# Kernel optimization log

Hardware: AMD Instinct MI355X
Metric: run time of the kernel (lower is better)

Reference implementation:

```python
import jax, jax.numpy as jnp
import numpy as np

M, NM, EM = 7, 1024, 32768        # modules, nodes/module, edges/module
N, E = M * NM, M * EM
F, D, H = 128, 64, 4              # node feats, hidden_channels, heads
HC = H * D


def setup_inputs() -> dict:
    key = jax.random.key(0)
    ks = jax.random.split(key, 20)
    x = jax.random.normal(ks[0], (N, F), jnp.float32)
    # intra-module edges; nodes of module m occupy [m*NM, (m+1)*NM)
    base = jnp.repeat(jnp.arange(M, dtype=jnp.int32) * NM, EM)
    src = base + jax.random.randint(ks[1], (E,), 0, NM, dtype=jnp.int32)
    dst = base + jax.random.randint(ks[2], (E,), 0, NM, dtype=jnp.int32)
    edge_index = jnp.stack([src, dst])
    module_assignments = jnp.repeat(jnp.arange(M, dtype=jnp.int32), NM)
    rn = lambda k, sh: jax.random.normal(k, sh, jnp.float32) * 0.05
    return dict(
        x=x, edge_index=edge_index, module_assignments=module_assignments,
        g1_w=rn(ks[3], (M, F, H, D)), g1_as=rn(ks[4], (M, H, D)), g1_ad=rn(ks[5], (M, H, D)),
        g1_b=jnp.zeros((M, HC), jnp.float32),
        g2_w=rn(ks[6], (M, HC, 1, D)), g2_as=rn(ks[7], (M, 1, D)), g2_ad=rn(ks[8], (M, 1, D)),
        g2_b=jnp.zeros((M, D), jnp.float32),
        sa_in_w=rn(ks[9], (M, 3 * D, D)), sa_in_b=jnp.zeros((M, 3 * D), jnp.float32),
        sa_out_w=rn(ks[10], (M, D, D)), sa_out_b=jnp.zeros((M, D), jnp.float32),
        ca_in_w=rn(ks[11], (3 * D, D)), ca_in_b=jnp.zeros((3 * D,), jnp.float32),
        ca_out_w=rn(ks[12], (D, D)), ca_out_b=jnp.zeros((D,), jnp.float32),
        fusion_w=jnp.ones((M,), jnp.float32) / M,
        fc_w=rn(ks[13], (M * D, D)), fc_b=jnp.zeros((D,), jnp.float32),
        c1_w=rn(ks[14], (D, D // 2)), c1_b=jnp.zeros((D // 2,), jnp.float32),
        c2_w=rn(ks[15], (D // 2, 2)), c2_b=jnp.zeros((2,), jnp.float32))


def _gat(x, src, dst, W, a_s, a_d, b, concat):
    # PyG-style GATConv (eval mode, add_self_loops=True). x:[NM,Fin], W:[Fin,h,c]
    h = jnp.einsum('nf,fhc->nhc', x, W)          # [NM,h,c]
    es = (h * a_s).sum(-1)                        # [NM,h]
    ed = (h * a_d).sum(-1)
    sl = jnp.arange(NM, dtype=src.dtype)
    s = jnp.concatenate([src, sl])                # add self-loops
    d = jnp.concatenate([dst, sl])
    e = jax.nn.leaky_relu(es[s] + ed[d], 0.2)     # [E+NM,h]
    mx = jax.ops.segment_max(e, d, num_segments=NM)
    ex = jnp.exp(e - mx[d])
    den = jax.ops.segment_sum(ex, d, num_segments=NM)
    alpha = ex / (den[d] + 1e-16)
    out = jax.ops.segment_sum(alpha[:, :, None] * h[s], d, num_segments=NM)  # [NM,h,c]
    out = out.reshape(NM, -1) if concat else out.mean(axis=1)
    return out + b


def _mha(x, in_w, in_b, out_w, out_b, nh):
    # torch nn.MultiheadAttention, batch_first, batch=1, eval mode
    L, d = x.shape
    dh = d // nh
    q, k, v = jnp.split(x @ in_w.T + in_b, 3, axis=-1)
    q = q.reshape(L, nh, dh); k = k.reshape(L, nh, dh); v = v.reshape(L, nh, dh)
    att = jax.nn.softmax(jnp.einsum('qhd,khd->hqk', q, k) * (1.0 / np.sqrt(dh)), axis=-1)
    o = jnp.einsum('hqk,khd->qhd', att, v).reshape(L, d)
    return o @ out_w.T + out_b


def _forward(x, edge_index, g1_w, g1_as, g1_ad, g1_b, g2_w, g2_as, g2_ad, g2_b,
             sa_in_w, sa_in_b, sa_out_w, sa_out_b, ca_in_w, ca_in_b, ca_out_w, ca_out_b,
             fusion_w, fc_w, fc_b, c1_w, c1_b, c2_w, c2_b):
    # per-module subgraph extraction + reindex: modules are contiguous node
    # blocks and edges are grouped per module, so mask/relabel is a reshape.
    ei = edge_index.reshape(2, M, EM)
    offs = (jnp.arange(M, dtype=ei.dtype) * NM)[:, None]
    src = ei[0] - offs                 # [M,EM] local indices
    dst = ei[1] - offs
    xm = x.reshape(M, NM, F)

    def per_module(xm_, s_, d_, g1w, g1a, g1d, g1b_, g2w_, g2a, g2d, g2b_, siw, sib, sow, sob):
        h = jax.nn.relu(_gat(xm_, s_, d_, g1w, g1a, g1d, g1b_, True))   # [NM,HC]
        h = jax.nn.relu(_gat(h, s_, d_, g2w_, g2a, g2d, g2b_, False))   # [NM,D]
        h = _mha(h, siw, sib, sow, sob, H)                              # module self-attention
        return h.mean(axis=0)                                            # [D]

    reps = jax.vmap(per_module)(xm, src, dst, g1_w, g1_as, g1_ad, g1_b,
                                g2_w, g2_as, g2_ad, g2_b,
                                sa_in_w, sa_in_b, sa_out_w, sa_out_b)    # [M,D]
    cross = _mha(reps, ca_in_w, ca_in_b, ca_out_w, ca_out_b, H)          # [M,D]
    w = jax.nn.softmax(fusion_w)
    fused = (cross * w[:, None]).reshape(1, M * D) @ fc_w + fc_b         # [1,D]
    out = jax.nn.relu(fused @ c1_w + c1_b) @ c2_w + c2_b                 # [1,2]
    return out, reps


def reference(x, edge_index, module_assignments, g1_w, g1_as, g1_ad, g1_b,
              g2_w, g2_as, g2_ad, g2_b, sa_in_w, sa_in_b, sa_out_w, sa_out_b,
              ca_in_w, ca_in_b, ca_out_w, ca_out_b, fusion_w, fc_w, fc_b,
              c1_w, c1_b, c2_w, c2_b):
    del module_assignments  # encoded as contiguous blocks of NM nodes per module
    return _forward(x, edge_index, g1_w, g1_as, g1_ad, g1_b, g2_w, g2_as, g2_ad, g2_b,
                    sa_in_w, sa_in_b, sa_out_w, sa_out_b, ca_in_w, ca_in_b, ca_out_w,
                    ca_out_b, fusion_w, fc_w, fc_b, c1_w, c1_b, c2_w, c2_b)
```

## Files before the change

### kernel.cpp

```cpp
#include <hip/hip_runtime.h>
#include <hip/hip_bf16.h>
#include <stdint.h>

#define MODS 7
#define NMOD 1024
#define EMOD 32768
#define NN (MODS*NMOD)
#define EE (MODS*EMOD)
#define KC2 4
#define G1B (MODS*16*4)
#define NCHUNK 32

typedef __hip_bfloat16 bf16;

static __device__ __forceinline__ float lrelu(float x){ return x > 0.f ? x : 0.2f*x; }
static __device__ __forceinline__ float bfu(unsigned short u){ return __uint_as_float(((unsigned)u) << 16); }
static __device__ __forceinline__ float2 f2fma(float2 a, float2 b, float2 c){
  return make_float2(fmaf(a.x,b.x,c.x), fmaf(a.y,b.y,c.y));
}

template<int K, int JT, bool TB, int RT, bool OBF, int SC, bool TRQ>
__device__ __forceinline__ void gemm_body(int b, const float* __restrict__ A,
    const float* __restrict__ B, const float* __restrict__ bias, void* __restrict__ Cv,
    const float* __restrict__ a_s, const float* __restrict__ a_d,
    float* __restrict__ es, float* __restrict__ ed) {
  constexpr int jt = JT/64;
  constexpr int rtiles = NMOD/RT;
  constexpr int RPT = RT/16;
  int ct = b % jt; b /= jt;
  int rt = b % rtiles; b /= rtiles;
  int m = b;
  int row0 = m*NMOD + rt*RT;
  int col0 = ct*64;
  __shared__ float Ast[32][RT+4];
  __shared__ float Bs[32][68];
  float acc[RPT][4] = {};
  int tid = threadIdx.x;
  int tr = (tid >> 4) * RPT;
  int tc = (tid & 15) * 4;
  const float* Bm = B + (size_t)m*K*JT;
  for (int k0 = 0; k0 < K; k0 += 32) {
    if constexpr (RT >= 32) {
      constexpr int ANUM = RT*32/1024;
      #pragma unroll
      for (int i = 0; i < ANUM; ++i) {
        int it = tid + i*256;
        int rr = it >> 3, kk0 = (it & 7)*4;
        float4 t = *(const float4*)&A[(size_t)(row0+rr)*K + k0 + kk0];
        Ast[kk0+0][rr] = t.x; Ast[kk0+1][rr] = t.y; Ast[kk0+2][rr] = t.z; Ast[kk0+3][rr] = t.w;
      }
    } else {
      if (tid < 128) {
        int rr = tid >> 3, kk0 = (tid & 7)*4;
        float4 t = *(const float4*)&A[(size_t)(row0+rr)*K + k0 + kk0];
        Ast[kk0+0][rr] = t.x; Ast[kk0+1][rr] = t.y; Ast[kk0+2][rr] = t.z; Ast[kk0+3][rr] = t.w;
      }
    }
    #pragma unroll
    for (int i = 0; i < 2; ++i) {
      int it = tid + i*256;
      if (!TB) {
        int kk = it >> 4, jj0 = (it & 15)*4;
        float4 t = *(const float4*)&Bm[(size_t)(k0+kk)*JT + col0 + jj0];
        Bs[kk][jj0] = t.x; Bs[kk][jj0+1] = t.y; Bs[kk][jj0+2] = t.z; Bs[kk][jj0+3] = t.w;
      } else {
        int jj = it >> 3, kk0 = (it & 7)*4;
        float4 t = *(const float4*)&Bm[(size_t)(col0+jj)*K + k0 + kk0];
        Bs[kk0+0][jj] = t.x; Bs[kk0+1][jj] = t.y; Bs[kk0+2][jj] = t.z; Bs[kk0+3][jj] = t.w;
      }
    }
    __syncthreads();
    #pragma unroll
    for (int kk = 0; kk < 32; ++kk) {
      float4 bv = *(const float4*)&Bs[kk][tc];
      float av[RPT];
      if constexpr (RPT == 4) {
        float4 t = *(const float4*)&Ast[kk][tr];
        av[0] = t.x; av[1] = t.y; av[2] = t.z; av[3] = t.w;
      } else if constexpr (RPT == 2) {
        av[0] = Ast[kk][tr]; av[1] = Ast[kk][tr+1];
      } else {
        av[0] = Ast[kk][tr];
      }
      #pragma unroll
      for (int i = 0; i < RPT; ++i) {
        acc[i][0] += av[i]*bv.x; acc[i][1] += av[i]*bv.y;
        acc[i][2] += av[i]*bv.z; acc[i][3] += av[i]*bv.w;
      }
    }
    __syncthreads();
  }
  float4 bb = {0,0,0,0};
  if (bias) bb = *(const float4*)&bias[m*JT + col0 + tc];
  #pragma unroll
  for (int i = 0; i < RPT; ++i) {
    float4 o = { acc[i][0]+bb.x, acc[i][1]+bb.y, acc[i][2]+bb.z, acc[i][3]+bb.w };
    if constexpr (TRQ) {
      float* Cp = (float*)Cv;
      size_t idx = ((size_t)(m*3 + ct)*NMOD + (rt*RT + tr + i))*64 + tc;
      *(float4*)&Cp[idx] = o;
    } else {
      size_t idx = (size_t)(row0+tr+i)*JT + col0 + tc;
      if constexpr (OBF) {
        bf16* Cp = (bf16*)Cv;
        bf16 tmp[4] = { __float2bfloat16(o.x), __float2bfloat16(o.y),
                        __float2bfloat16(o.z), __float2bfloat16(o.w) };
        *(uint2*)&Cp[idx] = *(const uint2*)tmp;
      } else {
        float* Cp = (float*)Cv;
        *(float4*)&Cp[idx] = o;
      }
    }
  }
  if constexpr (SC == 4) {
    int hh = ct;
    float4 as4 = *(const float4*)&a_s[(m*4 + hh)*64 + tc];
    float4 ad4 = *(const float4*)&a_d[(m*4 + hh)*64 + tc];
    #pragma unroll
    for (int i = 0; i < RPT; ++i) {
      float s = acc[i][0]*as4.x + acc[i][1]*as4.y + acc[i][2]*as4.z + acc[i][3]*as4.w;
      float d = acc[i][0]*ad4.x + acc[i][1]*ad4.y + acc[i][2]*ad4.z + acc[i][3]*ad4.w;
      #pragma unroll
      for (int off = 1; off < 16; off <<= 1) { s += __shfl_xor(s, off); d += __shfl_xor(d, off); }
      if ((tid & 15) == 0) {
        es[(row0+tr+i)*4 + hh] = s;
        ed[(row0+tr+i)*4 + hh] = d;
      }
    }
  }
  if constexpr (SC == 1) {
    float4 as4 = *(const float4*)&a_s[m*64 + tc];
    float4 ad4 = *(const float4*)&a_d[m*64 + tc];
    float s = acc[0][0]*as4.x + acc[0][1]*as4.y + acc[0][2]*as4.z + acc[0][3]*as4.w;
    float d = acc[0][0]*ad4.x + acc[0][1]*ad4.y + acc[0][2]*ad4.z + acc[0][3]*ad4.w;
    #pragma unroll
    for (int off = 1; off < 16; off <<= 1) { s += __shfl_xor(s, off); d += __shfl_xor(d, off); }
    if ((tid & 15) == 0) { es[row0+tr] = s; ed[row0+tr] = d; }
  }
}

__device__ __forceinline__ void hist_body(int mm, const int* __restrict__ dst,
                                          int* __restrict__ rs, int* __restrict__ rs2) {
  __shared__ int hc[NMOD];
  __shared__ int hws[4];
  int tid = threadIdx.x;
  hc[tid] = 0; hc[tid+256] = 0; hc[tid+512] = 0; hc[tid+768] = 0;
  __syncthreads();
  const int4* d4 = (const int4*)(dst + mm*EMOD);
  int base = mm*NMOD;
  for (int it = tid; it < EMOD/4; it += 256) {
    int4 d = d4[it];
    atomicAdd(&hc[d.x - base], 1); atomicAdd(&hc[d.y - base], 1);
    atomicAdd(&hc[d.z - base], 1); atomicAdd(&hc[d.w - base], 1);
  }
  __syncthreads();
  int lane = tid & 63, wid = tid >> 6;
  int i0 = tid*4;
  int v0 = hc[i0], v1 = hc[i0+1], v2 = hc[i0+2], v3 = hc[i0+3];
  int T = v0+v1+v2+v3;
  int X = T;
  #pragma unroll
  for (int off = 1; off < 64; off <<= 1) { int t = __shfl_up(X, off); if (lane >= off) X += t; }
  if (lane == 63) hws[wid] = X;
  __syncthreads();
  int woff = 0;
  #pragma unroll
  for (int w = 0; w < 4; ++w) if (w < wid) woff += hws[w];
  int ex = mm*EMOD + woff + X - T;
  int4 o = make_int4(ex, ex+v0, ex+v0+v1, ex+v0+v1+v2);
  *(int4*)&rs[base + i0]  = o;
  *(int4*)&rs2[base + i0] = o;
  if (mm == MODS-1 && tid == 255) rs[NN] = EE;
}

__global__ __launch_bounds__(256) void k_g1h(const float* __restrict__ x,
    const float* __restrict__ g1w, bf16* __restrict__ h1,
    const float* __restrict__ a_s, const float* __restrict__ a_d,
    float* __restrict__ es, float* __restrict__ ed,
    const int* __restrict__ dst, int* __restrict__ rs, int* __restrict__ rs2) {
  if (blockIdx.x < G1B)
    gemm_body<128,256,false,64,true,4,false>(blockIdx.x, x, g1w, nullptr, h1, a_s, a_d, es, ed);
  else
    hist_body(blockIdx.x - G1B, dst, rs, rs2);
}

__global__ __launch_bounds__(256) void k_g2s(const float* __restrict__ A,
    const float* __restrict__ B, bf16* __restrict__ h2,
    const float* __restrict__ a_s, const float* __restrict__ a_d,
    float* __restrict__ es, float* __restrict__ ed) {
  gemm_body<256,64,false,16,true,1,false>(blockIdx.x, A, B, nullptr, h2, a_s, a_d, es, ed);
}

__global__ __launch_bounds__(256) void k_gqkv(const float* __restrict__ A,
    const float* __restrict__ B, const float* __restrict__ bias, float* __restrict__ C) {
  gemm_body<64,192,true,64,false,0,true>(blockIdx.x, A, B, bias, C, nullptr, nullptr, nullptr, nullptr);
}

__global__ void k_fill(const int* __restrict__ src, const int* __restrict__ dst,
                       int* __restrict__ rs2, int* __restrict__ csr_src) {
  int e4 = blockIdx.x*256 + threadIdx.x;
  if (e4 < EE/4) {
    int4 s = ((const int4*)src)[e4];
    int4 d = ((const int4*)dst)[e4];
    csr_src[atomicAdd(&rs2[d.x], 1)] = s.x;
    csr_src[atomicAdd(&rs2[d.y], 1)] = s.y;
    csr_src[atomicAdd(&rs2[d.z], 1)] = s.z;
    csr_src[atomicAdd(&rs2[d.w], 1)] = s.w;
  }
}

__global__ __launch_bounds__(256) void k_agg4(const bf16* __restrict__ h,
    const float* __restrict__ es, const float* __restrict__ ed, const int* __restrict__ rs,
    const int* __restrict__ csr_src, const float* __restrict__ bias, float* __restrict__ out) {
  int wid = __builtin_amdgcn_readfirstlane(threadIdx.x >> 6);
  int n = blockIdx.x*4 + wid;
  int lane = threadIdx.x & 63;
  int hh = lane >> 4;
  int m = n >> 10;
  const unsigned short* hp = (const unsigned short*)h;
  float edv = ed[n*4 + hh];
  float p0 = __expf(lrelu(es[n*4 + hh] + edv));
  float den = p0;
  ushort4 v0 = *(const ushort4*)&hp[(size_t)n*256 + lane*4];
  float a0 = p0*bfu(v0.x), a1 = p0*bfu(v0.y), a2 = p0*bfu(v0.z), a3 = p0*bfu(v0.w);
  int beg = rs[n], end = rs[n+1];
  int i = beg;
  for (; i + 16 <= end; i += 16) {
    int ss[16]; ushort4 ww[16]; float qq[16];
    #pragma unroll
    for (int k = 0; k < 16; ++k) ss[k] = csr_src[i+k];
    #pragma unroll
    for (int k = 0; k < 16; ++k) ww[k] = *(const ushort4*)&hp[(size_t)ss[k]*256 + lane*4];
    #pragma unroll
    for (int k = 0; k < 16; ++k) qq[k] = __expf(lrelu(es[ss[k]*4 + hh] + edv));
    #pragma unroll
    for (int k = 0; k < 16; ++k) {
      den += qq[k];
      a0 += qq[k]*bfu(ww[k].x); a1 += qq[k]*bfu(ww[k].y);
      a2 += qq[k]*bfu(ww[k].z); a3 += qq[k]*bfu(ww[k].w);
    }
  }
  for (; i + 4 <= end; i += 4) {
    int ss[4]; ushort4 ww[4]; float qq[4];
    #pragma unroll
    for (int k = 0; k < 4; ++k) ss[k] = csr_src[i+k];
    #pragma unroll
    for (int k = 0; k < 4; ++k) ww[k] = *(const ushort4*)&hp[(size_t)ss[k]*256 + lane*4];
    #pragma unroll
    for (int k = 0; k < 4; ++k) qq[k] = __expf(lrelu(es[ss[k]*4 + hh] + edv));
    #pragma unroll
    for (int k = 0; k < 4; ++k) {
      den += qq[k];
      a0 += qq[k]*bfu(ww[k].x); a1 += qq[k]*bfu(ww[k].y);
      a2 += qq[k]*bfu(ww[k].z); a3 += qq[k]*bfu(ww[k].w);
    }
  }
  for (; i < end; ++i) {
    int s = csr_src[i];
    ushort4 w = *(const ushort4*)&hp[(size_t)s*256 + lane*4];
    float q = __expf(lrelu(es[s*4 + hh] + edv));
    den += q;
    a0 += q*bfu(w.x); a1 += q*bfu(w.y); a2 += q*bfu(w.z); a3 += q*bfu(w.w);
  }
  float inv = 1.f/den;
  float4 bb = *(const float4*)&bias[m*256 + lane*4];
  float4 o = { fmaxf(a0*inv + bb.x, 0.f), fmaxf(a1*inv + bb.y, 0.f),
               fmaxf(a2*inv + bb.z, 0.f), fmaxf(a3*inv + bb.w, 0.f) };
  *(float4*)&out[(size_t)n*256 + lane*4] = o;
}

__global__ __launch_bounds__(256) void k_agg1(const bf16* __restrict__ h,
    const float* __restrict__ es, const float* __restrict__ ed, const int* __restrict__ rs,
    const int* __restrict__ csr_src, const float* __restrict__ bias, float* __restrict__ out) {
  int wid = __builtin_amdgcn_readfirstlane(threadIdx.x >> 6);
  int n = blockIdx.x*4 + wid;
  int lane = threadIdx.x & 63;
  int m = n >> 10;
  float edv = ed[n];
  float p0 = __expf(lrelu(es[n] + edv));
  float den = p0;
  float acc = p0 * __bfloat162float(h[(size_t)n*64 + lane]);
  int beg = rs[n], end = rs[n+1];
  int i = beg;
  for (; i + 16 <= end; i += 16) {
    int ss[16]; float vv[16]; float qq[16];
    #pragma unroll
    for (int k = 0; k < 16; ++k) ss[k] = csr_src[i+k];
    #pragma unroll
    for (int k = 0; k < 16; ++k) vv[k] = __bfloat162float(h[(size_t)ss[k]*64 + lane]);
    #pragma unroll
    for (int k = 0; k < 16; ++k) qq[k] = __expf(lrelu(es[ss[k]] + edv));
    #pragma unroll
    for (int k = 0; k < 16; ++k) { den += qq[k]; acc += qq[k]*vv[k]; }
  }
  for (; i + 4 <= end; i += 4) {
    int ss[4]; float vv[4]; float qq[4];
    #pragma unroll
    for (int k = 0; k < 4; ++k) ss[k] = csr_src[i+k];
    #pragma unroll
    for (int k = 0; k < 4; ++k) vv[k] = __bfloat162float(h[(size_t)ss[k]*64 + lane]);
    #pragma unroll
    for (int k = 0; k < 4; ++k) qq[k] = __expf(lrelu(es[ss[k]] + edv));
    #pragma unroll
    for (int k = 0; k < 4; ++k) { den += qq[k]; acc += qq[k]*vv[k]; }
  }
  for (; i < end; ++i) {
    int s = csr_src[i];
    float q = __expf(lrelu(es[s] + edv));
    den += q;
    acc += q * __bfloat162float(h[(size_t)s*64 + lane]);
  }
  float v = acc/den + bias[m*64 + lane];
  out[(size_t)n*64 + lane] = fmaxf(v, 0.f);
}

__global__ __launch_bounds__(256) void k_attn(const float* __restrict__ qkv,
    float* __restrict__ pd, float* __restrict__ pacc) {
  int b = blockIdx.x;
  int kcg = b & (KC2-1); b /= KC2;
  int h = b & 3; b >>= 2;
  int qt = b & 15; int m = b >> 4;
  int lane = threadIdx.x & 63;
  int wu = __builtin_amdgcn_readfirstlane(threadIdx.x >> 6);
  int nl = qt*64 + lane;
  int n = m*NMOD + nl;
  float2 q2[8];
  const float* qrow = qkv + ((size_t)(m*3 + 0)*NMOD + nl)*64 + h*16;
  #pragma unroll
  for (int c = 0; c < 4; ++c) {
    float4 t = *(const float4*)(qrow + 4*c);
    q2[2*c]   = make_float2(t.x*0.25f, t.y*0.25f);
    q2[2*c+1] = make_float2(t.z*0.25f, t.w*0.25f);
  }
  int k0 = kcg*256 + wu*64;
  const float* kb = qkv + ((size_t)(m*3 + 1)*NMOD + k0)*64 + h*16;
  const float* vb = qkv + ((size_t)(m*3 + 2)*NMOD + k0)*64 + h*16;
  float den = 0.f;
  float2 acc2[8] = {};
  for (int jb = 0; jb < 64; jb += 4) {
    float2 kr[4][8], vr[4][8];
    #pragma unroll
    for (int r = 0; r < 4; ++r) {
      const float2* kp = (const float2*)(kb + (size_t)(jb+r)*64);
      const float2* vp = (const float2*)(vb + (size_t)(jb+r)*64);
      #pragma unroll
      for (int c = 0; c < 8; ++c) { kr[r][c] = kp[c]; vr[r][c] = vp[c]; }
    }
    #pragma unroll
    for (int r = 0; r < 4; ++r) {
      float2 d0 = {0,0}, d1 = {0,0};
      #pragma unroll
      for (int c = 0; c < 8; c += 2) { d0 = f2fma(q2[c], kr[r][c], d0); d1 = f2fma(q2[c+1], kr[r][c+1], d1); }
      float p = __expf((d0.x + d0.y) + (d1.x + d1.y));
      den += p;
      float2 pp = {p, p};
      #pragma unroll
      for (int c = 0; c < 8; ++c) acc2[c] = f2fma(pp, vr[r][c], acc2[c]);
    }
  }
  __shared__ float red[4][64][17];
  #pragma unroll
  for (int c = 0; c < 8; ++c) { red[wu][lane][2*c] = acc2[c].x; red[wu][lane][2*c+1] = acc2[c].y; }
  red[wu][lane][16] = den;
  __syncthreads();
  if (wu == 0) {
    size_t o = ((size_t)n*4 + h)*KC2 + kcg;
    pd[o] = red[0][lane][16] + red[1][lane][16] + red[2][lane][16] + red[3][lane][16];
    #pragma unroll
    for (int c = 0; c < 16; ++c)
      pacc[o*16 + c] = red[0][lane][c] + red[1][lane][c] + red[2][lane][c] + red[3][lane][c];
  }
}

__global__ __launch_bounds__(256) void k_comb(const float* __restrict__ pd,
    const float* __restrict__ pacc, float* __restrict__ partial) {
  int m = blockIdx.x >> 5, chunk = blockIdx.x & 31;
  __shared__ float part[4][64];
  int tid = threadIdx.x;
  int j = tid & 63, pp = tid >> 6;
  int h = j >> 4, c = j & 15;
  float s = 0.f;
  int base = m*NMOD + chunk*32;
  #pragma unroll 4
  for (int i = pp*8; i < pp*8 + 8; ++i) {
    int n = base + i;
    size_t o = ((size_t)n*4 + h)*KC2;
    float den = pd[o] + pd[o+1] + pd[o+2] + pd[o+3];
    float t = pacc[o*16 + c] + pacc[(o+1)*16 + c] + pacc[(o+2)*16 + c] + pacc[(o+3)*16 + c];
    s += t/den;
  }
  part[pp][j] = s;
  __syncthreads();
  if (pp == 0) partial[(size_t)blockIdx.x*64 + j] = part[0][j]+part[1][j]+part[2][j]+part[3][j];
}

__global__ __launch_bounds__(256) void k_final(const float* __restrict__ partial,
    const float* __restrict__ out_w, const float* __restrict__ out_b,
    const float* __restrict__ ca_in_w, const float* __restrict__ ca_in_b,
    const float* __restrict__ ca_out_w, const float* __restrict__ ca_out_b,
    const float* __restrict__ fusion_w, const float* __restrict__ fc_w,
    const float* __restrict__ fc_b, const float* __restrict__ c1_w,
    const float* __restrict__ c1_b, const float* __restrict__ c2_w,
    const float* __restrict__ c2_b, float* __restrict__ dout) {
  __shared__ float PR[7][64];
  __shared__ float R[7][64];
  __shared__ float QKV[7][192];
  __shared__ float SC[4][7][8];
  __shared__ float AL[4][7][8];
  __shared__ float O[7][64];
  __shared__ float CR[7][64];
  __shared__ float W[8];
  __shared__ float part[4][64];
  __shared__ float FU[64];
  __shared__ float HM[32];
  int tid = threadIdx.x, lane = tid & 63;
  {
    int j = tid & 63, g = tid >> 6;
    for (int m = g; m < 7; m += 4) {
      float s = 0.f;
      #pragma unroll
      for (int k = 0; k < NCHUNK; ++k) s += partial[(size_t)(m*NCHUNK + k)*64 + j];
      PR[m][j] = s * (1.f/NMOD);
    }
  }
  __syncthreads();
  {
    int sub = tid & 3, tt0 = tid >> 2;
    #pragma unroll
    for (int it = 0; it < 7; ++it) {
      int t = tt0 + it*64;
      int qi = t >> 6, j = t & 63;
      const float4* wr = (const float4*)&out_w[((size_t)qi*64 + j)*64 + sub*16];
      const float4* rr = (const float4*)&PR[qi][sub*16];
      float s = 0.f;
      #pragma unroll
      for (int c = 0; c < 4; ++c) {
        float4 a = rr[c], w4 = wr[c];
        s += a.x*w4.x + a.y*w4.y + a.z*w4.z + a.w*w4.w;
      }
      s += __shfl_xor(s, 1); s += __shfl_xor(s, 2);
      if (sub == 0) {
        float r = s + out_b[qi*64 + j];
        R[qi][j] = r;
        dout[2 + qi*64 + j] = r;
      }
    }
  }
  __syncthreads();
  {
    int sub = tid & 3, tt0 = tid >> 2;
    #pragma unroll 3
    for (int it = 0; it < 21; ++it) {
      int t = tt0 + it*64;
      int r = t/192, j = t - r*192;
      const float4* wr = (const float4*)&ca_in_w[j*64 + sub*16];
      const float4* rr = (const float4*)&R[r][sub*16];
      float s = 0.f;
      #pragma unroll
      for (int c = 0; c < 4; ++c) {
        float4 a = rr[c], w4 = wr[c];
        s += a.x*w4.x + a.y*w4.y + a.z*w4.z + a.w*w4.w;
      }
      s += __shfl_xor(s, 1); s += __shfl_xor(s, 2);
      if (sub == 0) QKV[r][j] = s + ca_in_b[j];
    }
    if (tid == 252) {
      float p[7]; float den = 0.f;
      #pragma unroll
      for (int i = 0; i < 7; ++i) { p[i] = __expf(fusion_w[i]); den += p[i]; }
      float inv = 1.f/den;
      #pragma unroll
      for (int i = 0; i < 7; ++i) W[i] = p[i]*inv;
    }
  }
  __syncthreads();
  if (tid < 196) {
    int hh = tid/49, rem = tid - hh*49, qi = rem/7, ki = rem - qi*7;
    float s = 0.f;
    #pragma unroll
    for (int c = 0; c < 16; ++c) s += QKV[qi][hh*16 + c]*QKV[ki][64 + hh*16 + c];
    SC[hh][qi][ki] = __expf(s*0.25f);
  }
  __syncthreads();
  if (tid < 28) {
    int hh = tid/7, qi = tid - hh*7;
    float den = 0.f;
    #pragma unroll
    for (int k = 0; k < 7; ++k) den += SC[hh][qi][k];
    float inv = 1.f/den;
    #pragma unroll
    for (int k = 0; k < 7; ++k) AL[hh][qi][k] = SC[hh][qi][k]*inv;
  }
  __syncthreads();
  for (int i = tid; i < 448; i += 256) {
    int qi = i >> 6, j = i & 63, hh = j >> 4;
    float s = 0.f;
    #pragma unroll
    for (int k = 0; k < 7; ++k) s += AL[hh][qi][k]*QKV[k][128 + j];
    O[qi][j] = s;
  }
  __syncthreads();
  {
    int sub = tid & 3, tt0 = tid >> 2;
    #pragma unroll
    for (int it = 0; it < 7; ++it) {
      int t = tt0 + it*64;
      int qi = t >> 6, j = t & 63;
      const float4* wr = (const float4*)&ca_out_w[j*64 + sub*16];
      const float4* orow = (const float4*)&O[qi][sub*16];
      float s = 0.f;
      #pragma unroll
      for (int c = 0; c < 4; ++c) {
        float4 a = orow[c], w4 = wr[c];
        s += a.x*w4.x + a.y*w4.y + a.z*w4.z + a.w*w4.w;
      }
      s += __shfl_xor(s, 1); s += __shfl_xor(s, 2);
      if (sub == 0) CR[qi][j] = s + ca_out_b[j];
    }
  }
  __syncthreads();
  {
    int w = tid >> 6;
    float s = 0.f;
    #pragma unroll 4
    for (int i = w*112; i < w*112 + 112; ++i)
      s += CR[i>>6][i&63]*W[i>>6]*fc_w[(size_t)i*64 + lane];
    part[w][lane] = s;
  }
  __syncthreads();
  if (tid < 64) FU[tid] = part[0][tid] + part[1][tid] + part[2][tid] + part[3][tid] + fc_b[tid];
  __syncthreads();
  if (tid < 128) {
    int sub = tid & 3, j = tid >> 2;
    float s = 0.f;
    #pragma unroll
    for (int c = 0; c < 16; ++c) { int k = sub*16 + c; s += FU[k]*c1_w[k*32 + j]; }
    s += __shfl_xor(s, 1); s += __shfl_xor(s, 2);
    if (sub == 0) HM[j] = fmaxf(s + c1_b[j], 0.f);
  }
  __syncthreads();
  if (tid < 2) {
    float s = c2_b[tid];
    #pragma unroll
    for (int k = 0; k < 32; ++k) s += HM[k]*c2_w[k*2 + tid];
    dout[tid] = s;
  }
}

extern "C" void kernel_launch(void* const* d_in, const int* in_sizes, int n_in,
                              void* d_out, int out_size, void* d_ws, size_t ws_size,
                              hipStream_t stream) {
  (void)in_sizes; (void)n_in; (void)out_size; (void)ws_size;
  const float* x       = (const float*)d_in[0];
  const int*   ei      = (const int*)d_in[1];
  const float* g1_w    = (const float*)d_in[3];
  const float* g1_as   = (const float*)d_in[4];
  const float* g1_ad   = (const float*)d_in[5];
  const float* g1_b    = (const float*)d_in[6];
  const float* g2_w    = (const float*)d_in[7];
  const float* g2_as   = (const float*)d_in[8];
  const float* g2_ad   = (const float*)d_in[9];
  const float* g2_b    = (const float*)d_in[10];
  const float* sa_in_w = (const float*)d_in[11];
  const float* sa_in_b = (const float*)d_in[12];
  const float* sa_out_w= (const float*)d_in[13];
  const float* sa_out_b= (const float*)d_in[14];
  const float* ca_in_w = (const float*)d_in[15];
  const float* ca_in_b = (const float*)d_in[16];
  const float* ca_out_w= (const float*)d_in[17];
  const float* ca_out_b= (const float*)d_in[18];
  const float* fusion_w= (const float*)d_in[19];
  const float* fc_w    = (const float*)d_in[20];
  const float* fc_b    = (const float*)d_in[21];
  const float* c1_w    = (const float*)d_in[22];
  const float* c1_b    = (const float*)d_in[23];
  const float* c2_w    = (const float*)d_in[24];
  const float* c2_b    = (const float*)d_in[25];
  float* dout = (float*)d_out;

  const int* src = ei;
  const int* dst = ei + EE;

  char* p = (char*)d_ws;
  int* rs      = (int*)p; p += (size_t)(NN+4)*sizeof(int);
  int* rs2     = (int*)p; p += (size_t)(NN+4)*sizeof(int);
  int* csr_src = (int*)p; p += (size_t)EE*sizeof(int);
  p = (char*)(((uintptr_t)p + 255) & ~(uintptr_t)255);
  float* h1f  = (float*)p; p += (size_t)NN*256*4;
  float* es1  = (float*)p; p += (size_t)NN*4*4;
  float* ed1  = (float*)p; p += (size_t)NN*4*4;
  float* gat1 = (float*)p; p += (size_t)NN*256*4;
  float* h2f  = (float*)p; p += (size_t)NN*64*4;
  float* es2  = (float*)p; p += (size_t)NN*4;
  float* ed2  = (float*)p; p += (size_t)NN*4;
  float* z    = (float*)p; p += (size_t)NN*64*4;
  float* pdbuf= (float*)p; p += (size_t)NN*4*KC2*4;
  float* partial = (float*)p; p += (size_t)MODS*NCHUNK*64*4;
  bf16* h1    = (bf16*)h1f;
  bf16* h2    = (bf16*)h2f;
  float* qkv  = h1f;
  float* pacc = gat1;
  float* pd   = pdbuf;

  k_g1h<<<G1B + MODS, 256, 0, stream>>>(x, g1_w, h1, g1_as, g1_ad, es1, ed1, dst, rs, rs2);
  k_fill<<<(EE/4+255)/256, 256, 0, stream>>>(src, dst, rs2, csr_src);
  k_agg4<<<NN/4, 256, 0, stream>>>(h1, es1, ed1, rs, csr_src, g1_b, gat1);
  k_g2s<<<MODS*64, 256, 0, stream>>>(gat1, g2_w, h2, g2_as, g2_ad, es2, ed2);
  k_agg1<<<NN/4, 256, 0, stream>>>(h2, es2, ed2, rs, csr_src, g2_b, z);
  k_gqkv<<<MODS*16*3, 256, 0, stream>>>(z, sa_in_w, sa_in_b, qkv);
  k_attn<<<MODS*16*4*KC2, 256, 0, stream>>>(qkv, pd, pacc);
  k_comb<<<MODS*NCHUNK, 256, 0, stream>>>(pd, pacc, partial);
  k_final<<<1, 256, 0, stream>>>(partial, sa_out_w, sa_out_b,
                                 ca_in_w, ca_in_b, ca_out_w, ca_out_b,
                                 fusion_w, fc_w, fc_b, c1_w, c1_b, c2_w, c2_b, dout);
}
```

Before: 136.8 us.

## Rewrite per-module self-attention with bf16 MFMA and fused mean reduction

Replaces the scalar FP32 self-attention kernel and its separate combine kernel with one kernel. It uses 16x16x32 bf16 MFMA instructions for both the QK^T scores and the P·V products, and reduces the per-query outputs straight into per-tile partial sums. The QKV GEMM now writes Q (pre-scaled) and K as bf16, and writes V transposed in bf16 to suit the MFMA operand layout. This removes one launch and the large pd/pacc intermediate buffers. In exchange, Q, K, V and the probabilities lose precision to bf16, softmax runs without max subtraction, and the strided transposed V stores are uncoalesced.

```diff
diff --git a/kernel.cpp b/kernel.cpp
--- a/kernel.cpp
+++ b/kernel.cpp
@@ -7,23 +7,24 @@
 #define EMOD 32768
 #define NN (MODS*NMOD)
 #define EE (MODS*EMOD)
-#define KC2 4
 #define G1B (MODS*16*4)
-#define NCHUNK 32
 
 typedef __hip_bfloat16 bf16;
+typedef __attribute__((ext_vector_type(8))) short short8;
+typedef __attribute__((ext_vector_type(4))) float f32x4;
 
 static __device__ __forceinline__ float lrelu(float x){ return x > 0.f ? x : 0.2f*x; }
 static __device__ __forceinline__ float bfu(unsigned short u){ return __uint_as_float(((unsigned)u) << 16); }
-static __device__ __forceinline__ float2 f2fma(float2 a, float2 b, float2 c){
-  return make_float2(fmaf(a.x,b.x,c.x), fmaf(a.y,b.y,c.y));
+static __device__ __forceinline__ unsigned short f2b(float x){
+  unsigned u = __float_as_uint(x);
+  return (unsigned short)((u + 0x7FFFu + ((u >> 16) & 1u)) >> 16);
 }
 
 template<int K, int JT, bool TB, int RT, bool OBF, int SC, bool TRQ>
 __device__ __forceinline__ void gemm_body(int b, const float* __restrict__ A,
     const float* __restrict__ B, const float* __restrict__ bias, void* __restrict__ Cv,
     const float* __restrict__ a_s, const float* __restrict__ a_d,
-    float* __restrict__ es, float* __restrict__ ed) {
+    float* __restrict__ es, float* __restrict__ ed, bf16* __restrict__ vT) {
   constexpr int jt = JT/64;
   constexpr int rtiles = NMOD/RT;
   constexpr int RPT = RT/16;
@@ -96,9 +97,21 @@
   for (int i = 0; i < RPT; ++i) {
     float4 o = { acc[i][0]+bb.x, acc[i][1]+bb.y, acc[i][2]+bb.z, acc[i][3]+bb.w };
     if constexpr (TRQ) {
-      float* Cp = (float*)Cv;
-      size_t idx = ((size_t)(m*3 + ct)*NMOD + (rt*RT + tr + i))*64 + tc;
-      *(float4*)&Cp[idx] = o;
+      int nodel = rt*RT + tr + i;
+      if (ct < 2) {
+        float s = (ct == 0) ? 0.25f : 1.0f;
+        bf16* qkb = (bf16*)Cv;
+        unsigned short tmp[4] = { f2b(o.x*s), f2b(o.y*s), f2b(o.z*s), f2b(o.w*s) };
+        *(uint2*)&qkb[((size_t)(m*2 + ct)*NMOD + nodel)*64 + tc] = *(const uint2*)tmp;
+      } else {
+        float vals[4] = {o.x, o.y, o.z, o.w};
+        #pragma unroll
+        for (int j = 0; j < 4; ++j) {
+          int cg = tc + j;
+          int hd = cg >> 4, ci = cg & 15;
+          ((unsigned short*)vT)[((size_t)(m*4 + hd)*16 + ci)*1024 + nodel] = f2b(vals[j]);
+        }
+      }
     } else {
       size_t idx = (size_t)(row0+tr+i)*JT + col0 + tc;
       if constexpr (OBF) {
@@ -179,7 +192,7 @@
     float* __restrict__ es, float* __restrict__ ed,
     const int* __restrict__ dst, int* __restrict__ rs, int* __restrict__ rs2) {
   if (blockIdx.x < G1B)
-    gemm_body<128,256,false,64,true,4,false>(blockIdx.x, x, g1w, nullptr, h1, a_s, a_d, es, ed);
+    gemm_body<128,256,false,64,true,4,false>(blockIdx.x, x, g1w, nullptr, h1, a_s, a_d, es, ed, nullptr);
   else
     hist_body(blockIdx.x - G1B, dst, rs, rs2);
 }
@@ -188,12 +201,13 @@
     const float* __restrict__ B, bf16* __restrict__ h2,
     const float* __restrict__ a_s, const float* __restrict__ a_d,
     float* __restrict__ es, float* __restrict__ ed) {
-  gemm_body<256,64,false,16,true,1,false>(blockIdx.x, A, B, nullptr, h2, a_s, a_d, es, ed);
+  gemm_body<256,64,false,16,true,1,false>(blockIdx.x, A, B, nullptr, h2, a_s, a_d, es, ed, nullptr);
 }
 
 __global__ __launch_bounds__(256) void k_gqkv(const float* __restrict__ A,
-    const float* __restrict__ B, const float* __restrict__ bias, float* __restrict__ C) {
-  gemm_body<64,192,true,64,false,0,true>(blockIdx.x, A, B, bias, C, nullptr, nullptr, nullptr, nullptr);
+    const float* __restrict__ B, const float* __restrict__ bias,
+    bf16* __restrict__ qkb, bf16* __restrict__ vT) {
+  gemm_body<64,192,true,64,false,0,true>(blockIdx.x, A, B, bias, qkb, nullptr, nullptr, nullptr, nullptr, vT);
 }
 
 __global__ void k_fill(const int* __restrict__ src, const int* __restrict__ dst,
@@ -314,84 +328,56 @@
   out[(size_t)n*64 + lane] = fmaxf(v, 0.f);
 }
 
-__global__ __launch_bounds__(256) void k_attn(const float* __restrict__ qkv,
-    float* __restrict__ pd, float* __restrict__ pacc) {
+__global__ __launch_bounds__(256) void k_mha(const bf16* __restrict__ qkb,
+    const bf16* __restrict__ vTb, float* __restrict__ partial) {
   int b = blockIdx.x;
-  int kcg = b & (KC2-1); b /= KC2;
-  int h = b & 3; b >>= 2;
-  int qt = b & 15; int m = b >> 4;
+  int qt = b & 63, m = b >> 6;
   int lane = threadIdx.x & 63;
-  int wu = __builtin_amdgcn_readfirstlane(threadIdx.x >> 6);
-  int nl = qt*64 + lane;
-  int n = m*NMOD + nl;
-  float2 q2[8];
-  const float* qrow = qkv + ((size_t)(m*3 + 0)*NMOD + nl)*64 + h*16;
+  int h = __builtin_amdgcn_readfirstlane(threadIdx.x >> 6);
+  int g = lane >> 4, q16 = lane & 15;
+  const unsigned short* qkp = (const unsigned short*)qkb;
+  const unsigned short* vp  = (const unsigned short*)vTb;
+  short8 zero8 = {};
+  short8 qfrag = zero8;
+  if (g < 2) qfrag = *(const short8*)&qkp[((size_t)(m*2 + 0)*NMOD + qt*16 + q16)*64 + h*16 + g*8];
+  f32x4 acc = {0.f, 0.f, 0.f, 0.f};
+  float dacc = 0.f;
+  int s0 = (q16 + ((g*2 + 0) << 4)) & 63;
+  int s1 = (q16 + ((g*2 + 1) << 4)) & 63;
+  #pragma unroll 2
+  for (int kt = 0; kt < 64; ++kt) {
+    short8 kfrag = zero8;
+    if (g < 2) kfrag = *(const short8*)&qkp[((size_t)(m*2 + 1)*NMOD + kt*16 + q16)*64 + h*16 + g*8];
+    f32x4 st = __builtin_amdgcn_mfma_f32_16x16x32_bf16(kfrag, qfrag, (f32x4){0.f,0.f,0.f,0.f}, 0, 0, 0);
+    float P0 = __expf(st[0]), P1 = __expf(st[1]), P2 = __expf(st[2]), P3 = __expf(st[3]);
+    dacc += (P0 + P1) + (P2 + P3);
+    float b0 = __shfl(P0, s0), b1 = __shfl(P1, s0), b2 = __shfl(P2, s0), b3 = __shfl(P3, s0);
+    float b4 = __shfl(P0, s1), b5 = __shfl(P1, s1), b6 = __shfl(P2, s1), b7 = __shfl(P3, s1);
+    short8 bfrag = zero8;
+    if (g < 2) {
+      bfrag[0] = (short)f2b(b0); bfrag[1] = (short)f2b(b1);
+      bfrag[2] = (short)f2b(b2); bfrag[3] = (short)f2b(b3);
+      bfrag[4] = (short)f2b(b4); bfrag[5] = (short)f2b(b5);
+      bfrag[6] = (short)f2b(b6); bfrag[7] = (short)f2b(b7);
+    }
+    short8 vfrag = zero8;
+    if (g < 2) vfrag = *(const short8*)&vp[((size_t)(m*4 + h)*16 + q16)*1024 + kt*16 + g*8];
+    acc = __builtin_amdgcn_mfma_f32_16x16x32_bf16(vfrag, bfrag, acc, 0, 0, 0);
+  }
+  float den = dacc;
+  den += __shfl_xor(den, 16);
+  den += __shfl_xor(den, 32);
+  float inv = 1.f / den;
+  float o0 = acc[0]*inv, o1 = acc[1]*inv, o2 = acc[2]*inv, o3 = acc[3]*inv;
   #pragma unroll
-  for (int c = 0; c < 4; ++c) {
-    float4 t = *(const float4*)(qrow + 4*c);
-    q2[2*c]   = make_float2(t.x*0.25f, t.y*0.25f);
-    q2[2*c+1] = make_float2(t.z*0.25f, t.w*0.25f);
-  }
-  int k0 = kcg*256 + wu*64;
-  const float* kb = qkv + ((size_t)(m*3 + 1)*NMOD + k0)*64 + h*16;
-  const float* vb = qkv + ((size_t)(m*3 + 2)*NMOD + k0)*64 + h*16;
-  float den = 0.f;
-  float2 acc2[8] = {};
-  for (int jb = 0; jb < 64; jb += 4) {
-    float2 kr[4][8], vr[4][8];
-    #pragma unroll
-    for (int r = 0; r < 4; ++r) {
-      const float2* kp = (const float2*)(kb + (size_t)(jb+r)*64);
-      const float2* vp = (const float2*)(vb + (size_t)(jb+r)*64);
-      #pragma unroll
-      for (int c = 0; c < 8; ++c) { kr[r][c] = kp[c]; vr[r][c] = vp[c]; }
-    }
-    #pragma unroll
-    for (int r = 0; r < 4; ++r) {
-      float2 d0 = {0,0}, d1 = {0,0};
-      #pragma unroll
-      for (int c = 0; c < 8; c += 2) { d0 = f2fma(q2[c], kr[r][c], d0); d1 = f2fma(q2[c+1], kr[r][c+1], d1); }
-      float p = __expf((d0.x + d0.y) + (d1.x + d1.y));
-      den += p;
-      float2 pp = {p, p};
-      #pragma unroll
-      for (int c = 0; c < 8; ++c) acc2[c] = f2fma(pp, vr[r][c], acc2[c]);
-    }
-  }
-  __shared__ float red[4][64][17];
-  #pragma unroll
-  for (int c = 0; c < 8; ++c) { red[wu][lane][2*c] = acc2[c].x; red[wu][lane][2*c+1] = acc2[c].y; }
-  red[wu][lane][16] = den;
-  __syncthreads();
-  if (wu == 0) {
-    size_t o = ((size_t)n*4 + h)*KC2 + kcg;
-    pd[o] = red[0][lane][16] + red[1][lane][16] + red[2][lane][16] + red[3][lane][16];
-    #pragma unroll
-    for (int c = 0; c < 16; ++c)
-      pacc[o*16 + c] = red[0][lane][c] + red[1][lane][c] + red[2][lane][c] + red[3][lane][c];
-  }
-}
-
-__global__ __launch_bounds__(256) void k_comb(const float* __restrict__ pd,
-    const float* __restrict__ pacc, float* __restrict__ partial) {
-  int m = blockIdx.x >> 5, chunk = blockIdx.x & 31;
-  __shared__ float part[4][64];
-  int tid = threadIdx.x;
-  int j = tid & 63, pp = tid >> 6;
-  int h = j >> 4, c = j & 15;
-  float s = 0.f;
-  int base = m*NMOD + chunk*32;
-  #pragma unroll 4
-  for (int i = pp*8; i < pp*8 + 8; ++i) {
-    int n = base + i;
-    size_t o = ((size_t)n*4 + h)*KC2;
-    float den = pd[o] + pd[o+1] + pd[o+2] + pd[o+3];
-    float t = pacc[o*16 + c] + pacc[(o+1)*16 + c] + pacc[(o+2)*16 + c] + pacc[(o+3)*16 + c];
-    s += t/den;
-  }
-  part[pp][j] = s;
-  __syncthreads();
-  if (pp == 0) partial[(size_t)blockIdx.x*64 + j] = part[0][j]+part[1][j]+part[2][j]+part[3][j];
+  for (int off = 1; off < 16; off <<= 1) {
+    o0 += __shfl_xor(o0, off); o1 += __shfl_xor(o1, off);
+    o2 += __shfl_xor(o2, off); o3 += __shfl_xor(o3, off);
+  }
+  if (q16 == 0) {
+    float* pp = &partial[((size_t)(m*64 + qt))*64 + h*16 + g*4];
+    pp[0] = o0; pp[1] = o1; pp[2] = o2; pp[3] = o3;
+  }
 }
 
 __global__ __launch_bounds__(256) void k_final(const float* __restrict__ partial,
@@ -415,12 +401,12 @@
   __shared__ float HM[32];
   int tid = threadIdx.x, lane = tid & 63;
   {
-    int j = tid & 63, g = tid >> 6;
-    for (int m = g; m < 7; m += 4) {
+    int j = tid & 63, gg = tid >> 6;
+    for (int mm = gg; mm < 7; mm += 4) {
       float s = 0.f;
-      #pragma unroll
-      for (int k = 0; k < NCHUNK; ++k) s += partial[(size_t)(m*NCHUNK + k)*64 + j];
-      PR[m][j] = s * (1.f/NMOD);
+      #pragma unroll 8
+      for (int k = 0; k < 64; ++k) s += partial[(size_t)(mm*64 + k)*64 + j];
+      PR[mm][j] = s * (1.f/NMOD);
     }
   }
   __syncthreads();
@@ -594,22 +580,20 @@
   float* es2  = (float*)p; p += (size_t)NN*4;
   float* ed2  = (float*)p; p += (size_t)NN*4;
   float* z    = (float*)p; p += (size_t)NN*64*4;
-  float* pdbuf= (float*)p; p += (size_t)NN*4*KC2*4;
-  float* partial = (float*)p; p += (size_t)MODS*NCHUNK*64*4;
+  bf16*  qkb  = (bf16*)p; p += (size_t)MODS*2*NMOD*64*sizeof(bf16);
+  bf16*  vTb  = (bf16*)p; p += (size_t)MODS*4*16*NMOD*sizeof(bf16);
+  p = (char*)(((uintptr_t)p + 255) & ~(uintptr_t)255);
+  float* partial = (float*)p; p += (size_t)MODS*64*64*4;
   bf16* h1    = (bf16*)h1f;
   bf16* h2    = (bf16*)h2f;
-  float* qkv  = h1f;
-  float* pacc = gat1;
-  float* pd   = pdbuf;
 
   k_g1h<<<G1B + MODS, 256, 0, stream>>>(x, g1_w, h1, g1_as, g1_ad, es1, ed1, dst, rs, rs2);
   k_fill<<<(EE/4+255)/256, 256, 0, stream>>>(src, dst, rs2, csr_src);
   k_agg4<<<NN/4, 256, 0, stream>>>(h1, es1, ed1, rs, csr_src, g1_b, gat1);
   k_g2s<<<MODS*64, 256, 0, stream>>>(gat1, g2_w, h2, g2_as, g2_ad, es2, ed2);
   k_agg1<<<NN/4, 256, 0, stream>>>(h2, es2, ed2, rs, csr_src, g2_b, z);
-  k_gqkv<<<MODS*16*3, 256, 0, stream>>>(z, sa_in_w, sa_in_b, qkv);
-  k_attn<<<MODS*16*4*KC2, 256, 0, stream>>>(qkv, pd, pacc);
-  k_comb<<<MODS*NCHUNK, 256, 0, stream>>>(pd, pacc, partial);
+  k_gqkv<<<MODS*16*3, 256, 0, stream>>>(z, sa_in_w, sa_in_b, qkb, vTb);
+  k_mha<<<MODS*64, 256, 0, stream>>>(qkb, vTb, partial);
   k_final<<<1, 256, 0, stream>>>(partial, sa_out_w, sa_out_b,
                                  ca_in_w, ca_in_b, ca_out_w, ca_out_b,
                                  fusion_w, fc_w, fc_b, c1_w, c1_b, c2_w, c2_b, dout);
```

Result: slower. 154.2 us (+12.7%).
